# Kernel optimization log

Measured on AMD Instinct MI355X. Metric: run time of the kernel, lower is better.

Reference implementation:

```python
import jax, jax.numpy as jnp
import numpy as np

B, N, D = 2048, 64, 128  # batch, num hist nodes (n-1), d_model
EPS = 1e-8


def setup_inputs() -> dict:
    key = jax.random.key(0)
    k1, k2, k3, k4, k5 = jax.random.split(key, 5)
    A_guide = jax.random.uniform(k1, (B, N, N), dtype=jnp.float32)  # nonneg for NMF
    X_guide = jax.random.normal(k2, (B, D, N), dtype=jnp.float32)
    x_new = jax.random.normal(k3, (B, 1, D), dtype=jnp.float32)
    U0 = jax.random.normal(k4, (B, N, N), dtype=jnp.float32)  # pre-softplus NMF init
    V0 = jax.random.normal(k5, (B, N, N), dtype=jnp.float32)
    return {"A_guide": A_guide, "X_guide": X_guide, "x_new": x_new, "U0": U0, "V0": V0}


def _nmf(A, U0, V0, n_iter=10):
    U = jax.nn.softplus(U0)
    V = jax.nn.softplus(V0)

    def step(carry, _):
        U, V = carry
        UT = jnp.swapaxes(U, 1, 2)
        V = V * (UT @ A) / (UT @ U @ V + EPS)
        VT = jnp.swapaxes(V, 1, 2)
        U = U * (A @ VT) / (U @ V @ VT + EPS)
        return (U, V), None

    (U, V), _ = jax.lax.scan(step, (U, V), None, length=n_iter)
    return U, V


def reference(A_guide, X_guide, x_new, U0, V0):
    d_model = X_guide.shape[1]
    n = X_guide.shape[2]
    # Step 1: deterministic NMF of historical adjacency
    U, V = _nmf(A_guide, U0, V0)
    # Step 2: orthogonal projection P = X X^T  (B, d, d)
    P = X_guide @ jnp.swapaxes(X_guide, 1, 2)
    # project new node feature: (B,1,d) @ (B,d,d) -> (B,d)
    x_p = (x_new @ P)[:, 0]
    # semantic attention: (B,1,n)
    attn_semantic = jnp.einsum('bd,bdn->bn', x_p, X_guide) / (d_model ** 0.5)
    # structural attention via UV reconstruction
    a = U @ V                                      # (B, n, n)
    x_p_rep = jnp.broadcast_to(x_p[:, None, :], (x_p.shape[0], n, x_p.shape[1]))
    x_p_UV = a @ x_p_rep                           # (B, n, d)
    attn_struct = x_p_UV @ X_guide                 # (B, n, n)
    fused = attn_semantic[:, None, :] * attn_struct  # broadcast (B,1,n)*(B,n,n)
    A_Tn = jax.nn.softmax(fused, axis=-1)
    return (A_Tn, x_p, U, V)
```

## Files before the change

kernel.cpp:

```cpp
#include <hip/hip_runtime.h>
#include <hip/hip_bf16.h>

#define EPS 1e-8f

typedef _Float16 half8 __attribute__((ext_vector_type(8)));
typedef _Float16 half4 __attribute__((ext_vector_type(4)));
typedef float f32x4 __attribute__((ext_vector_type(4)));

__device__ __forceinline__ float softplus_f(float x) {
    return fmaxf(x, 0.f) + log1pf(expf(-fabsf(x)));
}

__device__ __forceinline__ int swzh(int r, int c) {
    return r * 64 + ((((c >> 3) ^ (r & 7)) << 3) | (c & 7));
}

struct Frag {
    half8 h0, h1;
};

template <int CT>
__device__ __forceinline__ Frag load_strip(const _Float16* p0, const _Float16* p1) {
    Frag f;
    f.h0 = *(const half8*)(p0 + CT * 1024);
    f.h1 = *(const half8*)(p1 + CT * 1024);
    return f;
}

__device__ __forceinline__ void mfma_acc(const Frag& a, const Frag& b, f32x4& acc) {
    acc = __builtin_amdgcn_mfma_f32_16x16x32_f16(a.h0, b.h0, acc, 0, 0, 0);
    acc = __builtin_amdgcn_mfma_f32_16x16x32_f16(a.h1, b.h1, acc, 0, 0, 0);
}

struct NmfLds {
    _Float16 V_cm[4096];
    _Float16 U_rm[4096];
    _Float16 U_cm[4096];
    _Float16 V_rm[4096];
    union {
        _Float16 WZ[4096];
        float vp[4][64];
    } u;
};

__global__ __launch_bounds__(256, 4) void nmf_kernel(const float* __restrict__ Ag,
                                                     const float* __restrict__ U0,
                                                     const float* __restrict__ V0,
                                                     float* __restrict__ out,
                                                     float* __restrict__ ws) {
    __shared__ NmfLds S;
    const int b = blockIdx.x;
    const int tid = threadIdx.x;
    const int wave = tid >> 6;
    const int lane = tid & 63;
    const int lr = lane & 15;
    const int lk = lane >> 4;
    const int x = lr & 7;

    const float* Ab = Ag + (size_t)b * 4096;
    const float* Ub = U0 + (size_t)b * 4096;
    const float* Vb = V0 + (size_t)b * 4096;

    float Ureg[4][4];
    float VregT[4][4];

    const int sg0 = (lk ^ x) << 3;
    const int sg1 = ((lk + 4) ^ x) << 3;
    const _Float16* rUcm0 = S.U_cm + lr * 64 + sg0;
    const _Float16* rUcm1 = S.U_cm + lr * 64 + sg1;
    const _Float16* rVrm0 = S.V_rm + lr * 64 + sg0;
    const _Float16* rVrm1 = S.V_rm + lr * 64 + sg1;
    const _Float16* rWZ0 = S.u.WZ + lr * 64 + sg0;
    const _Float16* rWZ1 = S.u.WZ + lr * 64 + sg1;
    const int srow = (wave * 16 + lr) * 64;
    const _Float16* sUrm0 = S.U_rm + srow + sg0;
    const _Float16* sUrm1 = S.U_rm + srow + sg1;
    const _Float16* sUcm0 = S.U_cm + srow + sg0;
    const _Float16* sUcm1 = S.U_cm + srow + sg1;
    const _Float16* sVcm0 = S.V_cm + srow + sg0;
    const _Float16* sVcm1 = S.V_cm + srow + sg1;
    const _Float16* sVrm0 = S.V_rm + srow + sg0;
    const _Float16* sVrm1 = S.V_rm + srow + sg1;
    const int cg = ((wave * 2 + (lk >> 1)) ^ x) << 3;
    const int bg = (lk & 1) << 2;
    _Float16* wtrV = S.V_rm + lr * 64 + cg + bg;
    _Float16* wtrU = S.U_cm + lr * 64 + cg + bg;
    _Float16* wtrW = S.u.WZ + lr * 64 + cg + bg;
    const int g0 = lr >> 3;
    int oq[4];
#pragma unroll
    for (int q = 0; q < 4; ++q)
        oq[q] = (wave * 16 + lk * 4 + q) * 64 + ((g0 ^ ((lk * 4 + q) & 7)) << 3) + x;

#pragma unroll
    for (int t = 0; t < 4; ++t)
#pragma unroll
        for (int q = 0; q < 4; ++q) {
            const int r = wave * 16 + lk * 4 + q;
            const int c = t * 16 + lr;
            float a = Ab[r * 64 + c];
            S.U_rm[swzh(r, c)] = (_Float16)a;
            S.U_cm[swzh(c, r)] = (_Float16)a;
        }
    __syncthreads();
    const Frag arm = load_strip<0>(sUrm0, sUrm1);
    const Frag acm = load_strip<0>(sUcm0, sUcm1);
    __syncthreads();

#pragma unroll
    for (int t = 0; t < 4; ++t)
#pragma unroll
        for (int q = 0; q < 4; ++q) {
            const int r = wave * 16 + lk * 4 + q;
            const int c = t * 16 + lr;
            float uv = softplus_f(Ub[r * 64 + c]);
            Ureg[t][q] = uv;
            S.U_rm[swzh(r, c)] = (_Float16)uv;
            S.U_cm[swzh(c, r)] = (_Float16)uv;
            float vv = softplus_f(Vb[c * 64 + r]);
            VregT[t][q] = vv;
            S.V_cm[swzh(r, c)] = (_Float16)vv;
            S.V_rm[swzh(c, r)] = (_Float16)vv;
        }
    __syncthreads();

    const f32x4 zero4 = {0.f, 0.f, 0.f, 0.f};

    for (int it = 0; it < 10; ++it) {
        Frag ucself = load_strip<0>(sUcm0, sUcm1);
        f32x4 T1T[4] = {zero4, zero4, zero4, zero4};
        f32x4 W[4] = {zero4, zero4, zero4, zero4};
#define S1STEP(CT)                                \
    {                                             \
        Frag uct = load_strip<CT>(rUcm0, rUcm1);  \
        mfma_acc(acm, uct, T1T[CT]);              \
        mfma_acc(ucself, uct, W[CT]);             \
    }
        S1STEP(0) S1STEP(1) S1STEP(2) S1STEP(3)
#pragma unroll
        for (int t = 0; t < 4; ++t) {
            half4 p = {(_Float16)W[t][0], (_Float16)W[t][1], (_Float16)W[t][2],
                       (_Float16)W[t][3]};
            *(half4*)(wtrW + t * 1024) = p;
        }
        __syncthreads();

        Frag vtself = load_strip<0>(sVcm0, sVcm1);
        f32x4 WVT[4] = {zero4, zero4, zero4, zero4};
#define S2STEP(CT)                               \
    {                                            \
        Frag wct = load_strip<CT>(rWZ0, rWZ1);   \
        mfma_acc(vtself, wct, WVT[CT]);          \
    }
        S2STEP(0) S2STEP(1) S2STEP(2) S2STEP(3)

#pragma unroll
        for (int t = 0; t < 4; ++t) {
            half4 p;
#pragma unroll
            for (int q = 0; q < 4; ++q) {
                float v =
                    VregT[t][q] * T1T[t][q] * __builtin_amdgcn_rcpf(WVT[t][q] + EPS);
                VregT[t][q] = v;
                _Float16 h = (_Float16)v;
                p[q] = h;
                S.V_cm[oq[q] ^ (t << 4)] = h;
            }
            *(half4*)(wtrV + t * 1024) = p;
        }
        __syncthreads();

        Frag vrself = load_strip<0>(sVrm0, sVrm1);
        f32x4 T2[4] = {zero4, zero4, zero4, zero4};
        f32x4 Y[4] = {zero4, zero4, zero4, zero4};
#define S4STEP(CT)                                \
    {                                             \
        Frag vct = load_strip<CT>(rVrm0, rVrm1);  \
        mfma_acc(arm, vct, T2[CT]);               \
        mfma_acc(vrself, vct, Y[CT]);             \
    }
        S4STEP(0) S4STEP(1) S4STEP(2) S4STEP(3)
#pragma unroll
        for (int t = 0; t < 4; ++t) {
            half4 p = {(_Float16)Y[t][0], (_Float16)Y[t][1], (_Float16)Y[t][2],
                       (_Float16)Y[t][3]};
            *(half4*)(wtrW + t * 1024) = p;
        }
        __syncthreads();

        Frag urself = load_strip<0>(sUrm0, sUrm1);
        f32x4 ZV[4] = {zero4, zero4, zero4, zero4};
#define S5STEP(CT)                              \
    {                                           \
        Frag yct = load_strip<CT>(rWZ0, rWZ1);  \
        mfma_acc(urself, yct, ZV[CT]);          \
    }
        S5STEP(0) S5STEP(1) S5STEP(2) S5STEP(3)

#pragma unroll
        for (int t = 0; t < 4; ++t) {
            half4 p;
#pragma unroll
            for (int q = 0; q < 4; ++q) {
                float u = Ureg[t][q] * T2[t][q] * __builtin_amdgcn_rcpf(ZV[t][q] + EPS);
                Ureg[t][q] = u;
                _Float16 h = (_Float16)u;
                p[q] = h;
                S.U_rm[oq[q] ^ (t << 4)] = h;
            }
            *(half4*)(wtrU + t * 1024) = p;
        }
        __syncthreads();
    }

    {
        float part[4];
#pragma unroll
        for (int t = 0; t < 4; ++t) {
            float s = VregT[t][0] + VregT[t][1] + VregT[t][2] + VregT[t][3];
            s += __shfl_xor(s, 16);
            s += __shfl_xor(s, 32);
            part[t] = s;
        }
        if (lk == 0) {
#pragma unroll
            for (int t = 0; t < 4; ++t) S.u.vp[wave][t * 16 + lr] = part[t];
        }
    }
    __syncthreads();
#pragma unroll
    for (int q = 0; q < 4; ++q) {
        float p = 0.f;
#pragma unroll
        for (int t = 0; t < 4; ++t) {
            float vs = S.u.vp[0][t * 16 + lr] + S.u.vp[1][t * 16 + lr] +
                       S.u.vp[2][t * 16 + lr] + S.u.vp[3][t * 16 + lr];
            p += Ureg[t][q] * vs;
        }
        p += __shfl_xor(p, 1);
        p += __shfl_xor(p, 2);
        p += __shfl_xor(p, 4);
        p += __shfl_xor(p, 8);
        if (lr == 0) ws[(size_t)b * 64 + wave * 16 + lk * 4 + q] = p;
    }

    {
        float* Uout = out + 8650752 + (size_t)b * 4096;
        float* Vout = out + 17039360 + (size_t)b * 4096;
        const int rr = tid >> 2, qt = tid & 3;
        half8 u0 = *(const half8*)(S.U_rm + swzh(rr, qt * 16));
        half8 u1 = *(const half8*)(S.U_rm + swzh(rr, qt * 16 + 8));
        half8 v0 = *(const half8*)(S.V_rm + swzh(rr, qt * 16));
        half8 v1 = *(const half8*)(S.V_rm + swzh(rr, qt * 16 + 8));
        float4* Uo = (float4*)(Uout + rr * 64 + qt * 16);
        float4* Vo = (float4*)(Vout + rr * 64 + qt * 16);
        Uo[0] = {(float)u0[0], (float)u0[1], (float)u0[2], (float)u0[3]};
        Uo[1] = {(float)u0[4], (float)u0[5], (float)u0[6], (float)u0[7]};
        Uo[2] = {(float)u1[0], (float)u1[1], (float)u1[2], (float)u1[3]};
        Uo[3] = {(float)u1[4], (float)u1[5], (float)u1[6], (float)u1[7]};
        Vo[0] = {(float)v0[0], (float)v0[1], (float)v0[2], (float)v0[3]};
        Vo[1] = {(float)v0[4], (float)v0[5], (float)v0[6], (float)v0[7]};
        Vo[2] = {(float)v1[0], (float)v1[1], (float)v1[2], (float)v1[3]};
        Vo[3] = {(float)v1[4], (float)v1[5], (float)v1[6], (float)v1[7]};
    }
}

__global__ __launch_bounds__(256) void xp_kernel(const float* __restrict__ Xg,
                                                 const float* __restrict__ xn,
                                                 float* __restrict__ out,
                                                 const float* __restrict__ ws) {
    __shared__ float X[128 * 65];
    __shared__ float xnew[128];
    __shared__ float red[256];
    __shared__ float tbuf[64];
    __shared__ float xp[128];
    __shared__ float g[64];
    __shared__ float rs[64];
    __shared__ float gmax_s;
    const int b = blockIdx.x, tid = threadIdx.x;
    const float* Xb = Xg + (size_t)b * 8192;

    for (int idx = tid; idx < 2048; idx += 256) {
        float4 v = ((const float4*)Xb)[idx];
        int d = idx >> 4, n = (idx * 4) & 63;
        X[d * 65 + n + 0] = v.x;
        X[d * 65 + n + 1] = v.y;
        X[d * 65 + n + 2] = v.z;
        X[d * 65 + n + 3] = v.w;
    }
    if (tid < 32) {
        float4 v = ((const float4*)(xn + (size_t)b * 128))[tid];
        xnew[tid * 4 + 0] = v.x;
        xnew[tid * 4 + 1] = v.y;
        xnew[tid * 4 + 2] = v.z;
        xnew[tid * 4 + 3] = v.w;
    }
    if (tid >= 192) rs[tid - 192] = ws[(size_t)b * 64 + tid - 192];
    __syncthreads();
    {
        const int n = tid & 63, gi = tid >> 6;
        float p = 0.f;
        for (int d = gi * 32; d < gi * 32 + 32; ++d) p += xnew[d] * X[d * 65 + n];
        red[gi * 64 + n] = p;
    }
    __syncthreads();
    if (tid < 64) tbuf[tid] = red[tid] + red[64 + tid] + red[128 + tid] + red[192 + tid];
    __syncthreads();
    {
        const int d = tid & 127, h = tid >> 7;
        float p = 0.f;
        for (int n = h * 32; n < h * 32 + 32; ++n) p += X[d * 65 + n] * tbuf[n];
        red[h * 128 + d] = p;
    }
    __syncthreads();
    if (tid < 128) {
        float v = red[tid] + red[128 + tid];
        xp[tid] = v;
        out[8388608 + (size_t)b * 128 + tid] = v;
    }
    __syncthreads();
    {
        const int n = tid & 63, gi = tid >> 6;
        float p = 0.f;
        for (int d = gi * 32; d < gi * 32 + 32; ++d) p += xp[d] * X[d * 65 + n];
        red[gi * 64 + n] = p;
    }
    __syncthreads();
    if (tid < 64) {
        float s = red[tid] + red[64 + tid] + red[128 + tid] + red[192 + tid];
        g[tid] = s * s * 0.088388347648318447f;
    }
    __syncthreads();
    if (tid < 64) {
        float m = g[tid];
#pragma unroll
        for (int o = 1; o < 64; o <<= 1) m = fmaxf(m, __shfl_xor(m, o));
        if (tid == 0) gmax_s = m;
    }
    __syncthreads();
    const float gmax = gmax_s;
    const int i = tid >> 2, part = tid & 3;
    const float r = rs[i];
    float e[16];
    float sum = 0.f;
#pragma unroll
    for (int j = 0; j < 16; ++j) {
        e[j] = expf(r * (g[part * 16 + j] - gmax));
        sum += e[j];
    }
    sum += __shfl_xor(sum, 1);
    sum += __shfl_xor(sum, 2);
    const float inv = 1.f / sum;
    float* o = out + (size_t)b * 4096 + i * 64 + part * 16;
#pragma unroll
    for (int j = 0; j < 16; j += 4) {
        float4 v = {e[j] * inv, e[j + 1] * inv, e[j + 2] * inv, e[j + 3] * inv};
        ((float4*)o)[j >> 2] = v;
    }
}

extern "C" void kernel_launch(void* const* d_in, const int* in_sizes, int n_in,
                              void* d_out, int out_size, void* d_ws, size_t ws_size,
                              hipStream_t stream) {
    (void)in_sizes; (void)n_in; (void)out_size; (void)ws_size;
    const float* Ag = (const float*)d_in[0];
    const float* Xg = (const float*)d_in[1];
    const float* xn = (const float*)d_in[2];
    const float* U0 = (const float*)d_in[3];
    const float* V0 = (const float*)d_in[4];
    float* out = (float*)d_out;
    float* ws = (float*)d_ws;

    hipLaunchKernelGGL(nmf_kernel, dim3(2048), dim3(256), 0, stream, Ag, U0, V0, out, ws);
    hipLaunchKernelGGL(xp_kernel, dim3(2048), dim3(256), 0, stream, Xg, xn, out, ws);
}
```

Baseline: 155.5 us.

## Alias NMF LDS buffers to shrink shared memory and raise occupancy

Shared memory for the NMF kernel drops from five 8 KB half buffers to four. The W/Y scratch is aliased onto the V row-major and U column-major buffers, with extra barriers added so scratch reads finish before the buffers are overwritten. The launch-bounds minimum-blocks hint is also removed. The goal is more resident blocks per CU to hide latency, at the cost of two extra __syncthreads per iteration and different register allocation.

```diff
diff --git a/kernel.cpp b/kernel.cpp
--- a/kernel.cpp
+++ b/kernel.cpp
@@ -35,19 +35,18 @@
 struct NmfLds {
     _Float16 V_cm[4096];
     _Float16 U_rm[4096];
-    _Float16 U_cm[4096];
-    _Float16 V_rm[4096];
     union {
-        _Float16 WZ[4096];
+        _Float16 U_cm[4096];
         float vp[4][64];
-    } u;
+    } u2;
+    _Float16 VW[4096];
 };
 
-__global__ __launch_bounds__(256, 4) void nmf_kernel(const float* __restrict__ Ag,
-                                                     const float* __restrict__ U0,
-                                                     const float* __restrict__ V0,
-                                                     float* __restrict__ out,
-                                                     float* __restrict__ ws) {
+__global__ __launch_bounds__(256) void nmf_kernel(const float* __restrict__ Ag,
+                                                  const float* __restrict__ U0,
+                                                  const float* __restrict__ V0,
+                                                  float* __restrict__ out,
+                                                  float* __restrict__ ws) {
     __shared__ NmfLds S;
     const int b = blockIdx.x;
     const int tid = threadIdx.x;
@@ -66,26 +65,23 @@
 
     const int sg0 = (lk ^ x) << 3;
     const int sg1 = ((lk + 4) ^ x) << 3;
-    const _Float16* rUcm0 = S.U_cm + lr * 64 + sg0;
-    const _Float16* rUcm1 = S.U_cm + lr * 64 + sg1;
-    const _Float16* rVrm0 = S.V_rm + lr * 64 + sg0;
-    const _Float16* rVrm1 = S.V_rm + lr * 64 + sg1;
-    const _Float16* rWZ0 = S.u.WZ + lr * 64 + sg0;
-    const _Float16* rWZ1 = S.u.WZ + lr * 64 + sg1;
+    const _Float16* rB2_0 = S.u2.U_cm + lr * 64 + sg0;
+    const _Float16* rB2_1 = S.u2.U_cm + lr * 64 + sg1;
+    const _Float16* rB3_0 = S.VW + lr * 64 + sg0;
+    const _Float16* rB3_1 = S.VW + lr * 64 + sg1;
     const int srow = (wave * 16 + lr) * 64;
     const _Float16* sUrm0 = S.U_rm + srow + sg0;
     const _Float16* sUrm1 = S.U_rm + srow + sg1;
-    const _Float16* sUcm0 = S.U_cm + srow + sg0;
-    const _Float16* sUcm1 = S.U_cm + srow + sg1;
+    const _Float16* sUcm0 = S.u2.U_cm + srow + sg0;
+    const _Float16* sUcm1 = S.u2.U_cm + srow + sg1;
     const _Float16* sVcm0 = S.V_cm + srow + sg0;
     const _Float16* sVcm1 = S.V_cm + srow + sg1;
-    const _Float16* sVrm0 = S.V_rm + srow + sg0;
-    const _Float16* sVrm1 = S.V_rm + srow + sg1;
+    const _Float16* sB3_0 = S.VW + srow + sg0;
+    const _Float16* sB3_1 = S.VW + srow + sg1;
     const int cg = ((wave * 2 + (lk >> 1)) ^ x) << 3;
     const int bg = (lk & 1) << 2;
-    _Float16* wtrV = S.V_rm + lr * 64 + cg + bg;
-    _Float16* wtrU = S.U_cm + lr * 64 + cg + bg;
-    _Float16* wtrW = S.u.WZ + lr * 64 + cg + bg;
+    _Float16* trB3 = S.VW + lr * 64 + cg + bg;
+    _Float16* trB2 = S.u2.U_cm + lr * 64 + cg + bg;
     const int g0 = lr >> 3;
     int oq[4];
 #pragma unroll
@@ -99,11 +95,11 @@
             const int r = wave * 16 + lk * 4 + q;
             const int c = t * 16 + lr;
             float a = Ab[r * 64 + c];
-            S.U_rm[swzh(r, c)] = (_Float16)a;
-            S.U_cm[swzh(c, r)] = (_Float16)a;
-        }
-    __syncthreads();
-    const Frag arm = load_strip<0>(sUrm0, sUrm1);
+            S.VW[swzh(r, c)] = (_Float16)a;
+            S.u2.U_cm[swzh(c, r)] = (_Float16)a;
+        }
+    __syncthreads();
+    const Frag arm = load_strip<0>(sB3_0, sB3_1);
     const Frag acm = load_strip<0>(sUcm0, sUcm1);
     __syncthreads();
 
@@ -116,11 +112,10 @@
             float uv = softplus_f(Ub[r * 64 + c]);
             Ureg[t][q] = uv;
             S.U_rm[swzh(r, c)] = (_Float16)uv;
-            S.U_cm[swzh(c, r)] = (_Float16)uv;
+            S.u2.U_cm[swzh(c, r)] = (_Float16)uv;
             float vv = softplus_f(Vb[c * 64 + r]);
             VregT[t][q] = vv;
             S.V_cm[swzh(r, c)] = (_Float16)vv;
-            S.V_rm[swzh(c, r)] = (_Float16)vv;
         }
     __syncthreads();
 
@@ -132,7 +127,7 @@
         f32x4 W[4] = {zero4, zero4, zero4, zero4};
 #define S1STEP(CT)                                \
     {                                             \
-        Frag uct = load_strip<CT>(rUcm0, rUcm1);  \
+        Frag uct = load_strip<CT>(rB2_0, rB2_1);  \
         mfma_acc(acm, uct, T1T[CT]);              \
         mfma_acc(ucself, uct, W[CT]);             \
     }
@@ -141,7 +136,7 @@
         for (int t = 0; t < 4; ++t) {
             half4 p = {(_Float16)W[t][0], (_Float16)W[t][1], (_Float16)W[t][2],
                        (_Float16)W[t][3]};
-            *(half4*)(wtrW + t * 1024) = p;
+            *(half4*)(trB3 + t * 1024) = p;
         }
         __syncthreads();
 
@@ -149,10 +144,11 @@
         f32x4 WVT[4] = {zero4, zero4, zero4, zero4};
 #define S2STEP(CT)                               \
     {                                            \
-        Frag wct = load_strip<CT>(rWZ0, rWZ1);   \
+        Frag wct = load_strip<CT>(rB3_0, rB3_1); \
         mfma_acc(vtself, wct, WVT[CT]);          \
     }
         S2STEP(0) S2STEP(1) S2STEP(2) S2STEP(3)
+        __syncthreads();
 
 #pragma unroll
         for (int t = 0; t < 4; ++t) {
@@ -166,16 +162,16 @@
                 p[q] = h;
                 S.V_cm[oq[q] ^ (t << 4)] = h;
             }
-            *(half4*)(wtrV + t * 1024) = p;
-        }
-        __syncthreads();
-
-        Frag vrself = load_strip<0>(sVrm0, sVrm1);
+            *(half4*)(trB3 + t * 1024) = p;
+        }
+        __syncthreads();
+
+        Frag vrself = load_strip<0>(sB3_0, sB3_1);
         f32x4 T2[4] = {zero4, zero4, zero4, zero4};
         f32x4 Y[4] = {zero4, zero4, zero4, zero4};
 #define S4STEP(CT)                                \
     {                                             \
-        Frag vct = load_strip<CT>(rVrm0, rVrm1);  \
+        Frag vct = load_strip<CT>(rB3_0, rB3_1);  \
         mfma_acc(arm, vct, T2[CT]);               \
         mfma_acc(vrself, vct, Y[CT]);             \
     }
@@ -184,18 +180,19 @@
         for (int t = 0; t < 4; ++t) {
             half4 p = {(_Float16)Y[t][0], (_Float16)Y[t][1], (_Float16)Y[t][2],
                        (_Float16)Y[t][3]};
-            *(half4*)(wtrW + t * 1024) = p;
+            *(half4*)(trB2 + t * 1024) = p;
         }
         __syncthreads();
 
         Frag urself = load_strip<0>(sUrm0, sUrm1);
         f32x4 ZV[4] = {zero4, zero4, zero4, zero4};
-#define S5STEP(CT)                              \
-    {                                           \
-        Frag yct = load_strip<CT>(rWZ0, rWZ1);  \
-        mfma_acc(urself, yct, ZV[CT]);          \
+#define S5STEP(CT)                               \
+    {                                            \
+        Frag yct = load_strip<CT>(rB2_0, rB2_1); \
+        mfma_acc(urself, yct, ZV[CT]);           \
     }
         S5STEP(0) S5STEP(1) S5STEP(2) S5STEP(3)
+        __syncthreads();
 
 #pragma unroll
         for (int t = 0; t < 4; ++t) {
@@ -208,7 +205,7 @@
                 p[q] = h;
                 S.U_rm[oq[q] ^ (t << 4)] = h;
             }
-            *(half4*)(wtrU + t * 1024) = p;
+            *(half4*)(trB2 + t * 1024) = p;
         }
         __syncthreads();
     }
@@ -224,7 +221,7 @@
         }
         if (lk == 0) {
 #pragma unroll
-            for (int t = 0; t < 4; ++t) S.u.vp[wave][t * 16 + lr] = part[t];
+            for (int t = 0; t < 4; ++t) S.u2.vp[wave][t * 16 + lr] = part[t];
         }
     }
     __syncthreads();
@@ -233,8 +230,8 @@
         float p = 0.f;
 #pragma unroll
         for (int t = 0; t < 4; ++t) {
-            float vs = S.u.vp[0][t * 16 + lr] + S.u.vp[1][t * 16 + lr] +
-                       S.u.vp[2][t * 16 + lr] + S.u.vp[3][t * 16 + lr];
+            float vs = S.u2.vp[0][t * 16 + lr] + S.u2.vp[1][t * 16 + lr] +
+                       S.u2.vp[2][t * 16 + lr] + S.u2.vp[3][t * 16 + lr];
             p += Ureg[t][q] * vs;
         }
         p += __shfl_xor(p, 1);
@@ -250,8 +247,8 @@
         const int rr = tid >> 2, qt = tid & 3;
         half8 u0 = *(const half8*)(S.U_rm + swzh(rr, qt * 16));
         half8 u1 = *(const half8*)(S.U_rm + swzh(rr, qt * 16 + 8));
-        half8 v0 = *(const half8*)(S.V_rm + swzh(rr, qt * 16));
-        half8 v1 = *(const half8*)(S.V_rm + swzh(rr, qt * 16 + 8));
+        half8 v0 = *(const half8*)(S.VW + swzh(rr, qt * 16));
+        half8 v1 = *(const half8*)(S.VW + swzh(rr, qt * 16 + 8));
         float4* Uo = (float4*)(Uout + rr * 64 + qt * 16);
         float4* Vo = (float4*)(Vout + rr * 64 + qt * 16);
         Uo[0] = {(float)u0[0], (float)u0[1], (float)u0[2], (float)u0[3]};
```

Measured after the change: 187.5 us. 1.21x slower.

## Reassociate NMF denominators to drop two block barriers per iteration

Applied to the files above, without the earlier changes.

The NMF denominators are reassociated so the intermediate product (V^T U^T, or U^T V, in transposed layout) is computed per wave and kept in a wave-private scratch slice. It is no longer written to a shared WZ buffer that needs a block-wide barrier. This removes two __syncthreads per iteration, leaving two. The launch-bounds occupancy hint of 4 blocks is also dropped, which may change register allocation. The reassociation changes the fp16 rounding order of the intermediates.

```diff
diff --git a/kernel.cpp b/kernel.cpp
--- a/kernel.cpp
+++ b/kernel.cpp
@@ -38,16 +38,16 @@
     _Float16 U_cm[4096];
     _Float16 V_rm[4096];
     union {
-        _Float16 WZ[4096];
+        _Float16 scr[4096];
         float vp[4][64];
     } u;
 };
 
-__global__ __launch_bounds__(256, 4) void nmf_kernel(const float* __restrict__ Ag,
-                                                     const float* __restrict__ U0,
-                                                     const float* __restrict__ V0,
-                                                     float* __restrict__ out,
-                                                     float* __restrict__ ws) {
+__global__ __launch_bounds__(256) void nmf_kernel(const float* __restrict__ Ag,
+                                                  const float* __restrict__ U0,
+                                                  const float* __restrict__ V0,
+                                                  float* __restrict__ out,
+                                                  float* __restrict__ ws) {
     __shared__ NmfLds S;
     const int b = blockIdx.x;
     const int tid = threadIdx.x;
@@ -66,12 +66,14 @@
 
     const int sg0 = (lk ^ x) << 3;
     const int sg1 = ((lk + 4) ^ x) << 3;
+    const _Float16* rUrm0 = S.U_rm + lr * 64 + sg0;
+    const _Float16* rUrm1 = S.U_rm + lr * 64 + sg1;
     const _Float16* rUcm0 = S.U_cm + lr * 64 + sg0;
     const _Float16* rUcm1 = S.U_cm + lr * 64 + sg1;
+    const _Float16* rVcm0 = S.V_cm + lr * 64 + sg0;
+    const _Float16* rVcm1 = S.V_cm + lr * 64 + sg1;
     const _Float16* rVrm0 = S.V_rm + lr * 64 + sg0;
     const _Float16* rVrm1 = S.V_rm + lr * 64 + sg1;
-    const _Float16* rWZ0 = S.u.WZ + lr * 64 + sg0;
-    const _Float16* rWZ1 = S.u.WZ + lr * 64 + sg1;
     const int srow = (wave * 16 + lr) * 64;
     const _Float16* sUrm0 = S.U_rm + srow + sg0;
     const _Float16* sUrm1 = S.U_rm + srow + sg1;
@@ -79,18 +81,21 @@
     const _Float16* sUcm1 = S.U_cm + srow + sg1;
     const _Float16* sVcm0 = S.V_cm + srow + sg0;
     const _Float16* sVcm1 = S.V_cm + srow + sg1;
-    const _Float16* sVrm0 = S.V_rm + srow + sg0;
-    const _Float16* sVrm1 = S.V_rm + srow + sg1;
+    _Float16* scw = S.u.scr + wave * 1024;
+    const _Float16* sScr0 = scw + lr * 64 + sg0;
+    const _Float16* sScr1 = scw + lr * 64 + sg1;
+    const int g0 = lr >> 3;
+    int scq[4];
+#pragma unroll
+    for (int q = 0; q < 4; ++q)
+        scq[q] = (lk * 4 + q) * 64 + ((g0 ^ ((lk * 4 + q) & 7)) << 3) + x;
     const int cg = ((wave * 2 + (lk >> 1)) ^ x) << 3;
     const int bg = (lk & 1) << 2;
     _Float16* wtrV = S.V_rm + lr * 64 + cg + bg;
     _Float16* wtrU = S.U_cm + lr * 64 + cg + bg;
-    _Float16* wtrW = S.u.WZ + lr * 64 + cg + bg;
-    const int g0 = lr >> 3;
     int oq[4];
 #pragma unroll
-    for (int q = 0; q < 4; ++q)
-        oq[q] = (wave * 16 + lk * 4 + q) * 64 + ((g0 ^ ((lk * 4 + q) & 7)) << 3) + x;
+    for (int q = 0; q < 4; ++q) oq[q] = (wave * 16 + lk * 4 + q) * 64 + ((g0 ^ ((lk * 4 + q) & 7)) << 3) + x;
 
 #pragma unroll
     for (int t = 0; t < 4; ++t)
@@ -127,30 +132,27 @@
     const f32x4 zero4 = {0.f, 0.f, 0.f, 0.f};
 
     for (int it = 0; it < 10; ++it) {
-        Frag ucself = load_strip<0>(sUcm0, sUcm1);
+        Frag vtself = load_strip<0>(sVcm0, sVcm1);
+        f32x4 P[4] = {zero4, zero4, zero4, zero4};
+#define S1STEP(CT)                                 \
+    {                                              \
+        Frag urct = load_strip<CT>(rUrm0, rUrm1);  \
+        mfma_acc(vtself, urct, P[CT]);             \
+    }
+        S1STEP(0) S1STEP(1) S1STEP(2) S1STEP(3)
+#pragma unroll
+        for (int t = 0; t < 4; ++t)
+#pragma unroll
+            for (int q = 0; q < 4; ++q) scw[scq[q] ^ (t << 4)] = (_Float16)P[t][q];
+        Frag pf = load_strip<0>(sScr0, sScr1);
+
         f32x4 T1T[4] = {zero4, zero4, zero4, zero4};
-        f32x4 W[4] = {zero4, zero4, zero4, zero4};
-#define S1STEP(CT)                                \
+        f32x4 WVT[4] = {zero4, zero4, zero4, zero4};
+#define S2STEP(CT)                                \
     {                                             \
         Frag uct = load_strip<CT>(rUcm0, rUcm1);  \
         mfma_acc(acm, uct, T1T[CT]);              \
-        mfma_acc(ucself, uct, W[CT]);             \
-    }
-        S1STEP(0) S1STEP(1) S1STEP(2) S1STEP(3)
-#pragma unroll
-        for (int t = 0; t < 4; ++t) {
-            half4 p = {(_Float16)W[t][0], (_Float16)W[t][1], (_Float16)W[t][2],
-                       (_Float16)W[t][3]};
-            *(half4*)(wtrW + t * 1024) = p;
-        }
-        __syncthreads();
-
-        Frag vtself = load_strip<0>(sVcm0, sVcm1);
-        f32x4 WVT[4] = {zero4, zero4, zero4, zero4};
-#define S2STEP(CT)                               \
-    {                                            \
-        Frag wct = load_strip<CT>(rWZ0, rWZ1);   \
-        mfma_acc(vtself, wct, WVT[CT]);          \
+        mfma_acc(pf, uct, WVT[CT]);               \
     }
         S2STEP(0) S2STEP(1) S2STEP(2) S2STEP(3)
 
@@ -170,30 +172,27 @@
         }
         __syncthreads();
 
-        Frag vrself = load_strip<0>(sVrm0, sVrm1);
+        Frag urself = load_strip<0>(sUrm0, sUrm1);
+        f32x4 Q[4] = {zero4, zero4, zero4, zero4};
+#define S4STEP(CT)                                 \
+    {                                              \
+        Frag vcct = load_strip<CT>(rVcm0, rVcm1);  \
+        mfma_acc(urself, vcct, Q[CT]);             \
+    }
+        S4STEP(0) S4STEP(1) S4STEP(2) S4STEP(3)
+#pragma unroll
+        for (int t = 0; t < 4; ++t)
+#pragma unroll
+            for (int q = 0; q < 4; ++q) scw[scq[q] ^ (t << 4)] = (_Float16)Q[t][q];
+        Frag qf = load_strip<0>(sScr0, sScr1);
+
         f32x4 T2[4] = {zero4, zero4, zero4, zero4};
-        f32x4 Y[4] = {zero4, zero4, zero4, zero4};
-#define S4STEP(CT)                                \
+        f32x4 ZV[4] = {zero4, zero4, zero4, zero4};
+#define S5STEP(CT)                                \
     {                                             \
-        Frag vct = load_strip<CT>(rVrm0, rVrm1);  \
-        mfma_acc(arm, vct, T2[CT]);               \
-        mfma_acc(vrself, vct, Y[CT]);             \
-    }
-        S4STEP(0) S4STEP(1) S4STEP(2) S4STEP(3)
-#pragma unroll
-        for (int t = 0; t < 4; ++t) {
-            half4 p = {(_Float16)Y[t][0], (_Float16)Y[t][1], (_Float16)Y[t][2],
-                       (_Float16)Y[t][3]};
-            *(half4*)(wtrW + t * 1024) = p;
-        }
-        __syncthreads();
-
-        Frag urself = load_strip<0>(sUrm0, sUrm1);
-        f32x4 ZV[4] = {zero4, zero4, zero4, zero4};
-#define S5STEP(CT)                              \
-    {                                           \
-        Frag yct = load_strip<CT>(rWZ0, rWZ1);  \
-        mfma_acc(urself, yct, ZV[CT]);          \
+        Frag vrct = load_strip<CT>(rVrm0, rVrm1); \
+        mfma_acc(arm, vrct, T2[CT]);              \
+        mfma_acc(qf, vrct, ZV[CT]);               \
     }
         S5STEP(0) S5STEP(1) S5STEP(2) S5STEP(3)
 
```

Result: slower. 173.9 us (+11.9%).
